# Optimization experiments

Measured on AMD Instinct MI355X. Metric: run time of the kernel, lower is better.

Reference implementation:

```python
import jax, jax.numpy as jnp
import numpy as np

M = 262144          # rows of A == prod(out_shape) == 512*512
N = 262144          # cols of A == prod(x.shape)
NNZ = 8388608       # 32 nonzeros per row on average
OUT_SHAPE = (512, 512)


def setup_inputs() -> dict:
    key = jax.random.key(0)
    k1, k2, k3, k4 = jax.random.split(key, 4)
    A_rows = jax.random.randint(k1, (NNZ,), 0, M, dtype=jnp.int32)
    A_cols = jax.random.randint(k2, (NNZ,), 0, N, dtype=jnp.int32)
    A_vals = jax.random.normal(k3, (NNZ,), dtype=jnp.float32)
    x = jax.random.normal(k4, OUT_SHAPE, dtype=jnp.float32)
    return {"x": x, "A_vals": A_vals, "A_rows": A_rows, "A_cols": A_cols}


def reference(x, A_vals, A_rows, A_cols):
    # x.reshape(A.shape[1], 1); torch.sparse.mm(A, x); reshape(out_shape)
    xf = x.reshape(-1)                                   # [N]
    contrib = A_vals * jnp.take(xf, A_cols)              # [NNZ] gather + multiply
    y = jax.ops.segment_sum(contrib, A_rows, num_segments=M)  # scatter-add over rows
    return y.reshape(OUT_SHAPE).astype(jnp.float32)
```

## Files before the change

kernel.cpp:

```cpp
#include <hip/hip_runtime.h>


#define BINS         32
#define ROW_SHIFT    13
#define ROWS_PER_BIN 8192
#define ENT          4096
#define CUR_STRIDE   32
#define SL           16

typedef int   i32x4 __attribute__((ext_vector_type(4)));
typedef float f32x4 __attribute__((ext_vector_type(4)));


__global__ __launch_bounds__(256) void zero_out_kernel(float* __restrict__ y, int n) {
    int i = blockIdx.x * blockDim.x + threadIdx.x;
    if (i < n) y[i] = 0.0f;
}

__global__ __launch_bounds__(256) void spmv_coo_scatter(
    const float* __restrict__ vals, const int* __restrict__ rows,
    const int* __restrict__ cols, const float* __restrict__ x,
    float* __restrict__ y, int nnz)
{
    int i = (blockIdx.x * blockDim.x + threadIdx.x) * 4;
    if (i + 3 < nnz) {
        float4 v = *reinterpret_cast<const float4*>(vals + i);
        int4   r = *reinterpret_cast<const int4*>(rows + i);
        int4   c = *reinterpret_cast<const int4*>(cols + i);
        atomicAdd(&y[r.x], v.x * x[c.x]);
        atomicAdd(&y[r.y], v.y * x[c.y]);
        atomicAdd(&y[r.z], v.z * x[c.z]);
        atomicAdd(&y[r.w], v.w * x[c.w]);
    } else {
        for (; i < nnz; ++i) atomicAdd(&y[rows[i]], vals[i] * x[cols[i]]);
    }
}


__global__ __launch_bounds__(256, 4) void scatter2_kernel(
    const int*   __restrict__ rows, const int* __restrict__ cols,
    const float* __restrict__ vals, const float* __restrict__ x, int nnz,
    unsigned* __restrict__ gcur, unsigned cap,
    unsigned short* __restrict__ okeys, float* __restrict__ ocontrib)
{
    __shared__ unsigned cnt[BINS];
    __shared__ int      dstb[BINS];
    __shared__ unsigned cur2[BINS];
    __shared__ unsigned total_s;
    __shared__ unsigned short skey[ENT];
    __shared__ float          sval[ENT];
    __shared__ unsigned char  sbin[ENT];

    const int t = threadIdx.x;
    if (t < BINS) cnt[t] = 0u;
    __syncthreads();

    const int seg = blockIdx.x * ENT;

    int   rr[16];
    int   cc[16];
    float ff[16];

    if (seg + ENT <= nnz) {
        #pragma unroll
        for (int ch = 0; ch < 4; ++ch) {
            int base = seg + ch * 1024 + t * 4;
            i32x4 r4 = *reinterpret_cast<const i32x4*>(rows + base);
            i32x4 c4 = *reinterpret_cast<const i32x4*>(cols + base);
            f32x4 v4 = *reinterpret_cast<const f32x4*>(vals + base);
            rr[ch*4+0] = r4.x; cc[ch*4+0] = c4.x; ff[ch*4+0] = v4.x;
            rr[ch*4+1] = r4.y; cc[ch*4+1] = c4.y; ff[ch*4+1] = v4.y;
            rr[ch*4+2] = r4.z; cc[ch*4+2] = c4.z; ff[ch*4+2] = v4.z;
            rr[ch*4+3] = r4.w; cc[ch*4+3] = c4.w; ff[ch*4+3] = v4.w;
        }
        float xg[16];
        #pragma unroll
        for (int j = 0; j < 16; ++j) xg[j] = x[cc[j]];
        #pragma unroll
        for (int j = 0; j < 16; ++j) ff[j] *= xg[j];
    } else {
        #pragma unroll
        for (int ch = 0; ch < 4; ++ch) {
            #pragma unroll
            for (int j = 0; j < 4; ++j) {
                int idx = seg + ch * 1024 + t * 4 + j;
                if (idx < nnz) { rr[ch*4+j] = rows[idx]; cc[ch*4+j] = cols[idx]; ff[ch*4+j] = vals[idx]; }
                else           { rr[ch*4+j] = -1; cc[ch*4+j] = 0; ff[ch*4+j] = 0.0f; }
            }
        }
        #pragma unroll
        for (int j = 0; j < 16; ++j) if (rr[j] >= 0) ff[j] *= x[cc[j]];
    }

    #pragma unroll
    for (int j = 0; j < 16; ++j)
        if (rr[j] >= 0) atomicAdd(&cnt[rr[j] >> ROW_SHIFT], 1u);
    __syncthreads();

    if (t < BINS) {
        unsigned c = cnt[t];
        unsigned resv = atomicAdd(&gcur[t * CUR_STRIDE], c);
        unsigned v = c;
        #pragma unroll
        for (int d = 1; d < BINS; d <<= 1) {
            unsigned o = __shfl_up(v, d, 64);
            if (t >= d) v += o;
        }
        unsigned ls = v - c;
        cur2[t] = ls;
        dstb[t] = (int)resv - (int)ls;
        if (t == BINS - 1) total_s = v;
    }
    __syncthreads();

    #pragma unroll
    for (int j = 0; j < 16; ++j) {
        if (rr[j] >= 0) {
            int b = rr[j] >> ROW_SHIFT;
            unsigned p = atomicAdd(&cur2[b], 1u);
            skey[p] = (unsigned short)(rr[j] & (ROWS_PER_BIN - 1));
            sval[p] = ff[j];
            sbin[p] = (unsigned char)b;
        }
    }
    __syncthreads();

    const unsigned total = total_s;
    for (unsigned i = t; i < total; i += 256) {
        int b = sbin[i];
        unsigned off = (unsigned)(dstb[b] + (int)i);
        if (off < cap) {
            size_t dst = (size_t)b * cap + off;
            okeys[dst]    = skey[i];
            ocontrib[dst] = sval[i];
        }
    }
}

__global__ __launch_bounds__(512, 4) void accum2_kernel(
    const unsigned short* __restrict__ okeys, const float* __restrict__ ocontrib,
    const unsigned* __restrict__ gcur, unsigned cap,
    float* __restrict__ partials)
{
    __shared__ float acc[ROWS_PER_BIN];
    const int t   = threadIdx.x;
    const int bin = blockIdx.x / SL;
    const int sl  = blockIdx.x - bin * SL;

    float4 z = make_float4(0.f, 0.f, 0.f, 0.f);
    #pragma unroll
    for (int i = 0; i < ROWS_PER_BIN / (512 * 4); ++i)
        *reinterpret_cast<float4*>(&acc[(i * 512 + t) * 4]) = z;
    __syncthreads();

    unsigned count = gcur[bin * CUR_STRIDE];
    if (count > cap) count = cap;
    unsigned chunk = ((count + (unsigned)SL - 1u) / (unsigned)SL + 3u) & ~3u;
    unsigned lo = (unsigned)sl * chunk;
    unsigned hi = lo + chunk; if (hi > count) hi = count;

    const unsigned short* k = okeys    + (size_t)bin * cap;
    const float*          c = ocontrib + (size_t)bin * cap;

    unsigned i = lo + (unsigned)t * 4u;

    for (; i + 14339u < hi; i += 16384u) {
        ushort4 K[8];
        float4  C[8];
        #pragma unroll
        for (int j = 0; j < 8; ++j) K[j] = *reinterpret_cast<const ushort4*>(k + i + (unsigned)j * 2048u);
        #pragma unroll
        for (int j = 0; j < 8; ++j) C[j] = *reinterpret_cast<const float4*>(c + i + (unsigned)j * 2048u);
        #pragma unroll
        for (int j = 0; j < 8; ++j) {
            atomicAdd(&acc[K[j].x], C[j].x);
            atomicAdd(&acc[K[j].y], C[j].y);
            atomicAdd(&acc[K[j].z], C[j].z);
            atomicAdd(&acc[K[j].w], C[j].w);
        }
    }
    for (; i + 3u < hi; i += 2048u) {
        ushort4 k4 = *reinterpret_cast<const ushort4*>(k + i);
        float4  c4 = *reinterpret_cast<const float4*>(c + i);
        atomicAdd(&acc[k4.x], c4.x);
        atomicAdd(&acc[k4.y], c4.y);
        atomicAdd(&acc[k4.z], c4.z);
        atomicAdd(&acc[k4.w], c4.w);
    }
    for (; i < hi; ++i) atomicAdd(&acc[k[i]], c[i]);
    __syncthreads();

    float* p = partials + (size_t)blockIdx.x * ROWS_PER_BIN;
    #pragma unroll
    for (int i2 = 0; i2 < ROWS_PER_BIN / (512 * 4); ++i2) {
        int l = (i2 * 512 + t) * 4;
        *reinterpret_cast<float4*>(p + l) = *reinterpret_cast<const float4*>(&acc[l]);
    }
}

__global__ __launch_bounds__(256) void reduce2_kernel(
    const float* __restrict__ partials, float* __restrict__ y, int out_size)
{
    int r0 = (blockIdx.x * 256 + threadIdx.x) * 4;
    if (r0 >= out_size) return;
    int bin = r0 >> ROW_SHIFT, local = r0 & (ROWS_PER_BIN - 1);
    const float* p = partials + ((size_t)bin * SL) * ROWS_PER_BIN + local;
    float4 s = make_float4(0.f, 0.f, 0.f, 0.f);
    #pragma unroll
    for (int j = 0; j < SL; ++j) {
        float4 v = *reinterpret_cast<const float4*>(p + (size_t)j * ROWS_PER_BIN);
        s.x += v.x; s.y += v.y; s.z += v.z; s.w += v.w;
    }
    *reinterpret_cast<float4*>(y + r0) = s;
}

extern "C" void kernel_launch(void* const* d_in, const int* in_sizes, int n_in,
                              void* d_out, int out_size, void* d_ws, size_t ws_size,
                              hipStream_t stream) {
    const float* x    = (const float*)d_in[0];
    const float* vals = (const float*)d_in[1];
    const int*   rows = (const int*)d_in[2];
    const int*   cols = (const int*)d_in[3];
    float* y = (float*)d_out;

    const int nnz  = in_sizes[1];
    const int bins = (out_size + ROWS_PER_BIN - 1) / ROWS_PER_BIN;

    unsigned cap = (unsigned)(nnz / (bins > 0 ? bins : 1)) + 16384u;
    cap = (cap + 3u) & ~3u;

    auto align256 = [](size_t v) { return (v + 255) & ~(size_t)255; };

    size_t off_contrib  = 0;
    size_t off_keys     = align256(off_contrib + (size_t)BINS * cap * 4);
    size_t off_partials = align256(off_keys + (size_t)BINS * cap * 2);
    size_t off_gcur     = align256(off_partials + (size_t)BINS * SL * ROWS_PER_BIN * 4);
    size_t need         = align256(off_gcur + (size_t)BINS * CUR_STRIDE * 4);

    const bool ok = (bins == BINS) && (need <= ws_size) && (nnz > 0) &&
                    (out_size == BINS * ROWS_PER_BIN);

    if (!ok) {
        zero_out_kernel<<<(out_size + 255) / 256, 256, 0, stream>>>(y, out_size);
        spmv_coo_scatter<<<(nnz + 1023) / 1024, 256, 0, stream>>>(vals, rows, cols, x, y, nnz);
        return;
    }

    char* w = (char*)d_ws;
    float*          ocontrib = (float*)(w + off_contrib);
    unsigned short* okeys    = (unsigned short*)(w + off_keys);
    float*          partials = (float*)(w + off_partials);
    unsigned*       gcur     = (unsigned*)(w + off_gcur);

    hipMemsetAsync(gcur, 0, (size_t)BINS * CUR_STRIDE * 4, stream);

    scatter2_kernel<<<(nnz + ENT - 1) / ENT, 256, 0, stream>>>(
        rows, cols, vals, x, nnz, gcur, cap, okeys, ocontrib);
    accum2_kernel<<<BINS * SL, 512, 0, stream>>>(okeys, ocontrib, gcur, cap, partials);
    reduce2_kernel<<<(out_size / 4 + 255) / 256, 256, 0, stream>>>(partials, y, out_size);
}
```

Before: 220.8 us.

## Use finer row bins and accumulate each bin in one block directly into output

Row bins are halved to 4096 rows (64 bins), and each bin is accumulated by a single 1024-thread block that writes its shared-memory histogram straight to y. This removes the sliced partial buffers and the separate reduction kernel, along with their global memory traffic and one launch. In exchange, the accumulate stage runs only 64 blocks, far fewer than the number of compute units, so each block streams a whole bin serially and parallelism drops.

```diff
diff --git a/kernel.cpp b/kernel.cpp
--- a/kernel.cpp
+++ b/kernel.cpp
@@ -1,12 +1,11 @@
 #include <hip/hip_runtime.h>
 
 
-#define BINS         32
-#define ROW_SHIFT    13
-#define ROWS_PER_BIN 8192
+#define BINS         64
+#define ROW_SHIFT    12
+#define ROWS_PER_BIN 4096
 #define ENT          4096
 #define CUR_STRIDE   32
-#define SL           16
 
 typedef int   i32x4 __attribute__((ext_vector_type(4)));
 typedef float f32x4 __attribute__((ext_vector_type(4)));
@@ -137,40 +136,33 @@
     }
 }
 
-__global__ __launch_bounds__(512, 4) void accum2_kernel(
+__global__ __launch_bounds__(1024, 4) void accum_y_kernel(
     const unsigned short* __restrict__ okeys, const float* __restrict__ ocontrib,
     const unsigned* __restrict__ gcur, unsigned cap,
-    float* __restrict__ partials)
+    float* __restrict__ y)
 {
     __shared__ float acc[ROWS_PER_BIN];
     const int t   = threadIdx.x;
-    const int bin = blockIdx.x / SL;
-    const int sl  = blockIdx.x - bin * SL;
-
-    float4 z = make_float4(0.f, 0.f, 0.f, 0.f);
-    #pragma unroll
-    for (int i = 0; i < ROWS_PER_BIN / (512 * 4); ++i)
-        *reinterpret_cast<float4*>(&acc[(i * 512 + t) * 4]) = z;
+    const int bin = blockIdx.x;
+
+    *reinterpret_cast<float4*>(&acc[t * 4]) = make_float4(0.f, 0.f, 0.f, 0.f);
     __syncthreads();
 
     unsigned count = gcur[bin * CUR_STRIDE];
     if (count > cap) count = cap;
-    unsigned chunk = ((count + (unsigned)SL - 1u) / (unsigned)SL + 3u) & ~3u;
-    unsigned lo = (unsigned)sl * chunk;
-    unsigned hi = lo + chunk; if (hi > count) hi = count;
 
     const unsigned short* k = okeys    + (size_t)bin * cap;
     const float*          c = ocontrib + (size_t)bin * cap;
 
-    unsigned i = lo + (unsigned)t * 4u;
-
-    for (; i + 14339u < hi; i += 16384u) {
+    unsigned i = (unsigned)t * 4u;
+
+    for (; i + 28675u < count; i += 32768u) {
         ushort4 K[8];
         float4  C[8];
         #pragma unroll
-        for (int j = 0; j < 8; ++j) K[j] = *reinterpret_cast<const ushort4*>(k + i + (unsigned)j * 2048u);
-        #pragma unroll
-        for (int j = 0; j < 8; ++j) C[j] = *reinterpret_cast<const float4*>(c + i + (unsigned)j * 2048u);
+        for (int j = 0; j < 8; ++j) K[j] = *reinterpret_cast<const ushort4*>(k + i + (unsigned)j * 4096u);
+        #pragma unroll
+        for (int j = 0; j < 8; ++j) C[j] = *reinterpret_cast<const float4*>(c + i + (unsigned)j * 4096u);
         #pragma unroll
         for (int j = 0; j < 8; ++j) {
             atomicAdd(&acc[K[j].x], C[j].x);
@@ -179,7 +171,7 @@
             atomicAdd(&acc[K[j].w], C[j].w);
         }
     }
-    for (; i + 3u < hi; i += 2048u) {
+    for (; i + 3u < count; i += 4096u) {
         ushort4 k4 = *reinterpret_cast<const ushort4*>(k + i);
         float4  c4 = *reinterpret_cast<const float4*>(c + i);
         atomicAdd(&acc[k4.x], c4.x);
@@ -187,31 +179,11 @@
         atomicAdd(&acc[k4.z], c4.z);
         atomicAdd(&acc[k4.w], c4.w);
     }
-    for (; i < hi; ++i) atomicAdd(&acc[k[i]], c[i]);
-    __syncthreads();
-
-    float* p = partials + (size_t)blockIdx.x * ROWS_PER_BIN;
-    #pragma unroll
-    for (int i2 = 0; i2 < ROWS_PER_BIN / (512 * 4); ++i2) {
-        int l = (i2 * 512 + t) * 4;
-        *reinterpret_cast<float4*>(p + l) = *reinterpret_cast<const float4*>(&acc[l]);
-    }
-}
-
-__global__ __launch_bounds__(256) void reduce2_kernel(
-    const float* __restrict__ partials, float* __restrict__ y, int out_size)
-{
-    int r0 = (blockIdx.x * 256 + threadIdx.x) * 4;
-    if (r0 >= out_size) return;
-    int bin = r0 >> ROW_SHIFT, local = r0 & (ROWS_PER_BIN - 1);
-    const float* p = partials + ((size_t)bin * SL) * ROWS_PER_BIN + local;
-    float4 s = make_float4(0.f, 0.f, 0.f, 0.f);
-    #pragma unroll
-    for (int j = 0; j < SL; ++j) {
-        float4 v = *reinterpret_cast<const float4*>(p + (size_t)j * ROWS_PER_BIN);
-        s.x += v.x; s.y += v.y; s.z += v.z; s.w += v.w;
-    }
-    *reinterpret_cast<float4*>(y + r0) = s;
+    for (; i < count; ++i) atomicAdd(&acc[k[i]], c[i]);
+    __syncthreads();
+
+    *reinterpret_cast<float4*>(y + (size_t)bin * ROWS_PER_BIN + t * 4) =
+        *reinterpret_cast<const float4*>(&acc[t * 4]);
 }
 
 extern "C" void kernel_launch(void* const* d_in, const int* in_sizes, int n_in,
@@ -233,8 +205,7 @@
 
     size_t off_contrib  = 0;
     size_t off_keys     = align256(off_contrib + (size_t)BINS * cap * 4);
-    size_t off_partials = align256(off_keys + (size_t)BINS * cap * 2);
-    size_t off_gcur     = align256(off_partials + (size_t)BINS * SL * ROWS_PER_BIN * 4);
+    size_t off_gcur     = align256(off_keys + (size_t)BINS * cap * 2);
     size_t need         = align256(off_gcur + (size_t)BINS * CUR_STRIDE * 4);
 
     const bool ok = (bins == BINS) && (need <= ws_size) && (nnz > 0) &&
@@ -249,13 +220,11 @@
     char* w = (char*)d_ws;
     float*          ocontrib = (float*)(w + off_contrib);
     unsigned short* okeys    = (unsigned short*)(w + off_keys);
-    float*          partials = (float*)(w + off_partials);
     unsigned*       gcur     = (unsigned*)(w + off_gcur);
 
     hipMemsetAsync(gcur, 0, (size_t)BINS * CUR_STRIDE * 4, stream);
 
     scatter2_kernel<<<(nnz + ENT - 1) / ENT, 256, 0, stream>>>(
         rows, cols, vals, x, nnz, gcur, cap, okeys, ocontrib);
-    accum2_kernel<<<BINS * SL, 512, 0, stream>>>(okeys, ocontrib, gcur, cap, partials);
-    reduce2_kernel<<<(out_size / 4 + 255) / 256, 256, 0, stream>>>(partials, y, out_size);
-}
+    accum_y_kernel<<<BINS, 1024, 0, stream>>>(okeys, ocontrib, gcur, cap, y);
+}
```

New measurement: 342.6 us. +55.2%, slower.
